# Kernel optimization log

Measured on AMD Instinct MI355X. Metric: run time of the kernel, lower is better.

## Reference

```python
import jax, jax.numpy as jnp
import numpy as np

B, N, D = 16, 4096, 512   # batch, channels, d_model
R, K = 64, 128            # regions, channels per region


def setup_inputs() -> dict:
    key = jax.random.key(0)
    k1, k2, k3 = jax.random.split(key, 3)
    x = jax.random.normal(k1, (B, N, D), dtype=jnp.float32)
    region_indices = jax.random.randint(k2, (R, K), 0, N)
    W = jax.random.normal(k3, (1, D), dtype=jnp.float32) * (1.0 / np.sqrt(D))
    b = jnp.zeros((1,), dtype=jnp.float32)
    return {"x": x, "region_indices": region_indices, "W": W, "b": b}


def reference(x, region_indices, W, b):
    # Gather all regions at once: [B, R, K, D]
    xr = x[:, region_indices, :]
    # Tiny linear scorer 512 -> 1: [B, R, K]
    score = jnp.einsum('brkd,d->brk', xr, W[0]) + b[0]
    # Softmax over the K channels of each region
    attn = jax.nn.softmax(score, axis=-1)
    # Attention-weighted sum over region channels: [B, R, D]
    return jnp.einsum('brk,brkd->brd', attn, xr)
```

## Files before the change

### kernel.cpp

```cpp
#include <hip/hip_runtime.h>
#include <math.h>

constexpr int B = 16;
constexpr int N = 4096;
constexpr int D = 512;
constexpr int R = 64;
constexpr int K = 128;
constexpr int WAVES = 4;
constexpr int KPW = K / WAVES;

__global__ __launch_bounds__(256) void regional_attn_fused(
    const float* __restrict__ x,
    const int*   __restrict__ idx,
    const float* __restrict__ W,
    float* __restrict__ out)
{
    const int br   = blockIdx.x;
    const int b    = br / R;
    const int r    = br % R;
    const int tid  = threadIdx.x;
    const int lane = tid & 63;
    const int wave = tid >> 6;

    __shared__ int   s_idx[K];
    __shared__ float s_O[WAVES][D];
    __shared__ float s_m[WAVES];
    __shared__ float s_l[WAVES];

    if (tid < K) s_idx[tid] = idx[r * K + tid];

    const float4* W4 = (const float4*)W;
    const float4  w0 = W4[lane];
    const float4  w1 = W4[lane + 64];

    __syncthreads();

    const float* xb = x + (size_t)b * N * D;
    const int kbase = wave * KPW;

    float  m = -INFINITY;
    float  l = 0.0f;
    float4 O0 = make_float4(0.f, 0.f, 0.f, 0.f);
    float4 O1 = make_float4(0.f, 0.f, 0.f, 0.f);

    const float4* row = (const float4*)(xb + (size_t)s_idx[kbase] * D);
    float4 a0 = row[lane];
    float4 a1 = row[lane + 64];

    #pragma unroll 2
    for (int kk = 0; kk < KPW; ++kk) {
        float4 b0 = a0, b1 = a1;
        if (kk + 1 < KPW) {
            const float4* nrow = (const float4*)(xb + (size_t)s_idx[kbase + kk + 1] * D);
            a0 = nrow[lane];
            a1 = nrow[lane + 64];
        }
        float p = b0.x * w0.x + b0.y * w0.y + b0.z * w0.z + b0.w * w0.w
                + b1.x * w1.x + b1.y * w1.y + b1.z * w1.z + b1.w * w1.w;
        #pragma unroll
        for (int off = 1; off < 64; off <<= 1)
            p += __shfl_xor(p, off, 64);
        float m_new  = fmaxf(m, p);
        float alpha  = __expf(m - m_new);
        float e      = __expf(p - m_new);
        m = m_new;
        l = l * alpha + e;
        O0.x = O0.x * alpha + e * b0.x;
        O0.y = O0.y * alpha + e * b0.y;
        O0.z = O0.z * alpha + e * b0.z;
        O0.w = O0.w * alpha + e * b0.w;
        O1.x = O1.x * alpha + e * b1.x;
        O1.y = O1.y * alpha + e * b1.y;
        O1.z = O1.z * alpha + e * b1.z;
        O1.w = O1.w * alpha + e * b1.w;
    }

    ((float4*)&s_O[wave][0])[lane]      = O0;
    ((float4*)&s_O[wave][0])[lane + 64] = O1;
    if (lane == 0) { s_m[wave] = m; s_l[wave] = l; }
    __syncthreads();

    const float M  = fmaxf(fmaxf(s_m[0], s_m[1]), fmaxf(s_m[2], s_m[3]));
    const float e0 = __expf(s_m[0] - M);
    const float e1 = __expf(s_m[1] - M);
    const float e2 = __expf(s_m[2] - M);
    const float e3 = __expf(s_m[3] - M);
    const float denom = s_l[0] * e0 + s_l[1] * e1 + s_l[2] * e2 + s_l[3] * e3;
    const float inv = 1.0f / denom;

    const int d = 2 * tid;
    float ox = s_O[0][d]     * e0 + s_O[1][d]     * e1
             + s_O[2][d]     * e2 + s_O[3][d]     * e3;
    float oy = s_O[0][d + 1] * e0 + s_O[1][d + 1] * e1
             + s_O[2][d + 1] * e2 + s_O[3][d + 1] * e3;

    float2* out2 = (float2*)(out + ((size_t)b * R + r) * D);
    out2[tid] = make_float2(ox * inv, oy * inv);
}

extern "C" void kernel_launch(void* const* d_in, const int* in_sizes, int n_in,
                              void* d_out, int out_size, void* d_ws, size_t ws_size,
                              hipStream_t stream) {
    const float* x    = (const float*)d_in[0];
    const int*   idx  = (const int*)d_in[1];
    const float* W    = (const float*)d_in[2];
    float* out = (float*)d_out;

    dim3 grid(B * R);
    dim3 block(256);
    regional_attn_fused<<<grid, block, 0, stream>>>(x, idx, W, out);
}
```

Measured before the change: 200.1 us.

## Double waves per block and remap blocks so each XCD handles whole batches

Raises the block from 4 to 8 waves, so each wave processes half as many gathered rows and more loads are in flight per region. Block indices are remapped so all regions of two batches land on the same XCD, aiming for cache reuse of repeated gathered rows. The final merge loops over 8 partial softmax states, which adds shared-memory work and per-wave reduction overhead. The remap assumes round-robin dispatch of blocks across 8 XCDs.

```diff
diff --git a/kernel.cpp b/kernel.cpp
--- a/kernel.cpp
+++ b/kernel.cpp
@@ -6,18 +6,21 @@
 constexpr int D = 512;
 constexpr int R = 64;
 constexpr int K = 128;
-constexpr int WAVES = 4;
+constexpr int WAVES = 8;
 constexpr int KPW = K / WAVES;
 
-__global__ __launch_bounds__(256) void regional_attn_fused(
+__global__ __launch_bounds__(512, 8) void regional_attn_fused(
     const float* __restrict__ x,
     const int*   __restrict__ idx,
     const float* __restrict__ W,
     float* __restrict__ out)
 {
-    const int br   = blockIdx.x;
-    const int b    = br / R;
-    const int r    = br % R;
+    const int v    = blockIdx.x;
+    const int xcd  = v & 7;
+    const int slot = v >> 3;
+    const int b    = xcd * 2 + (slot >> 6);
+    const int r    = slot & 63;
+
     const int tid  = threadIdx.x;
     const int lane = tid & 63;
     const int wave = tid >> 6;
@@ -80,22 +83,24 @@
     if (lane == 0) { s_m[wave] = m; s_l[wave] = l; }
     __syncthreads();
 
-    const float M  = fmaxf(fmaxf(s_m[0], s_m[1]), fmaxf(s_m[2], s_m[3]));
-    const float e0 = __expf(s_m[0] - M);
-    const float e1 = __expf(s_m[1] - M);
-    const float e2 = __expf(s_m[2] - M);
-    const float e3 = __expf(s_m[3] - M);
-    const float denom = s_l[0] * e0 + s_l[1] * e1 + s_l[2] * e2 + s_l[3] * e3;
+    float M = s_m[0];
+    #pragma unroll
+    for (int w = 1; w < WAVES; ++w) M = fmaxf(M, s_m[w]);
+    float ew[WAVES];
+    float denom = 0.0f;
+    #pragma unroll
+    for (int w = 0; w < WAVES; ++w) {
+        ew[w] = __expf(s_m[w] - M);
+        denom += s_l[w] * ew[w];
+    }
     const float inv = 1.0f / denom;
 
-    const int d = 2 * tid;
-    float ox = s_O[0][d]     * e0 + s_O[1][d]     * e1
-             + s_O[2][d]     * e2 + s_O[3][d]     * e3;
-    float oy = s_O[0][d + 1] * e0 + s_O[1][d + 1] * e1
-             + s_O[2][d + 1] * e2 + s_O[3][d + 1] * e3;
+    const int d = tid;
+    float o = 0.0f;
+    #pragma unroll
+    for (int w = 0; w < WAVES; ++w) o += s_O[w][d] * ew[w];
 
-    float2* out2 = (float2*)(out + ((size_t)b * R + r) * D);
-    out2[tid] = make_float2(ox * inv, oy * inv);
+    out[((size_t)b * R + r) * D + d] = o * inv;
 }
 
 extern "C" void kernel_launch(void* const* d_in, const int* in_sizes, int n_in,
@@ -107,6 +112,6 @@
     float* out = (float*)d_out;
 
     dim3 grid(B * R);
-    dim3 block(256);
+    dim3 block(512);
     regional_attn_fused<<<grid, block, 0, stream>>>(x, idx, W, out);
 }
```

New measurement: 195.9 us. 2.1% less time.
